# Optimization experiments

Hardware: AMD Instinct MI355X
Metric: run time of the kernel (lower is better)

Reference implementation:

```python
import jax, jax.numpy as jnp
import numpy as np


def _ln(x, w, b, eps):
    mu = jnp.mean(x, axis=-1, keepdims=True)
    var = jnp.mean((x - mu) ** 2, axis=-1, keepdims=True)
    return (x - mu) * jax.lax.rsqrt(var + eps) * w + b


def _conv(x, w, stride, groups):
    # x: (N, C, H, W), w: (O, C/groups, kh, kw), VALID padding, no bias
    return jax.lax.conv_general_dilated(
        x, w, window_strides=(stride, stride), padding='VALID',
        dimension_numbers=('NCHW', 'OIHW', 'NCHW'), feature_group_count=groups)


def setup_inputs() -> dict:
    key = jax.random.key(0)
    ks = jax.random.split(key, 8)
    B, Hp, Wp = 16, 56, 56
    d_c, d_v, H = 768, 768, 12
    t, kvp = 2, 4
    dh, dvh = d_c // H, d_v // H
    s = 0.02
    return {
        'x': jax.random.normal(ks[0], (B, Hp * Wp, d_c), jnp.float32),
        'patches_h': Hp,
        'patches_w': Wp,
        'norm_w': jnp.ones((d_c,), jnp.float32),
        'norm_b': jnp.zeros((d_c,), jnp.float32),
        'qkv_w': jax.random.normal(ks[1], (3 * d_c, d_c), jnp.float32) * s,
        'qkv_b': jnp.zeros((3 * d_c,), jnp.float32),
        'pool_q_w': jax.random.normal(ks[2], (dh, 1, t, t), jnp.float32) * s,
        'pool_k_w': jax.random.normal(ks[3], (dh, 1, kvp, kvp), jnp.float32) * s,
        'pool_v_w': jax.random.normal(ks[4], (dvh, dh, kvp, kvp), jnp.float32) * s,
        'normq_w': jnp.ones((dh,), jnp.float32),
        'normq_b': jnp.zeros((dh,), jnp.float32),
        'normk_w': jnp.ones((dh,), jnp.float32),
        'normk_b': jnp.zeros((dh,), jnp.float32),
        'normv_w': jnp.ones((dvh,), jnp.float32),
        'normv_b': jnp.zeros((dvh,), jnp.float32),
        'proj_w': jax.random.normal(ks[5], (d_v, d_v), jnp.float32) * s,
        'proj_b': jnp.zeros((d_v,), jnp.float32),
    }


def reference(x, patches_h, patches_w, norm_w, norm_b, qkv_w, qkv_b,
              pool_q_w, pool_k_w, pool_v_w, normq_w, normq_b,
              normk_w, normk_b, normv_w, normv_b, proj_w, proj_b):
    B, N_c, d_c = x.shape
    dh = pool_q_w.shape[0]
    H = d_c // dh
    dvh = pool_v_w.shape[0]
    d_v = dvh * H
    t = pool_q_w.shape[-1]
    kvp = pool_k_w.shape[-1]
    scale = dh ** -0.5

    xn = _ln(x, norm_w, norm_b, 1e-6)
    qkv = xn @ qkv_w.T + qkv_b                          # (B, N_c, 3*d_c)
    qkv = qkv.reshape(B, N_c, 3, H, dh).transpose(2, 0, 3, 1, 4)
    q, k, v = qkv[0], qkv[1], qkv[2]                     # (B, H, N_c, dh)

    def to_maps(a):
        return a.reshape(B * H, patches_h, patches_w, dh).transpose(0, 3, 1, 2)

    q = _conv(to_maps(q), pool_q_w, t, dh)               # (B*H, dh, Hp/t, Wp/t)
    k = _conv(to_maps(k), pool_k_w, kvp, dh)
    v = _conv(to_maps(v), pool_v_w, kvp, 1)              # (B*H, dvh, ., .)
    N_v = q.shape[-2] * q.shape[-1]
    N_kv = k.shape[-2] * k.shape[-1]

    # NOTE: raw row-major reshape, exactly matching torch's .reshape semantics
    q = _ln(q.reshape(B, H, N_v, dh), normq_w, normq_b, 1e-5)
    k = _ln(k.reshape(B, H, N_kv, dh), normk_w, normk_b, 1e-5)
    v = _ln(v.reshape(B, H, N_kv, dvh), normv_w, normv_b, 1e-5)

    attn = jax.nn.softmax(jnp.einsum('bhnd,bhmd->bhnm', q * scale, k), axis=-1)
    out = jnp.einsum('bhnm,bhmd->bhnd', attn, v)         # (B, H, N_v, dvh)
    out = out.transpose(0, 2, 1, 3).reshape(B, N_v, d_v)
    return out @ proj_w.T + proj_b
```

## Files before the change

kernel.cpp:

```cpp
#include <hip/hip_runtime.h>
#include <hip/hip_bf16.h>

using short8 = __attribute__((ext_vector_type(8))) short;
using f32x4  = __attribute__((ext_vector_type(4))) float;

#define DEVI __device__ __forceinline__
#define SWZ(byte, row) ((unsigned)(byte) ^ ((((unsigned)(row)) & 7u) << 4))

DEVI unsigned short f2bf(float f){
  unsigned int u = __float_as_uint(f);
  unsigned int r = (u + 0x7fffu + ((u >> 16) & 1u)) >> 16;
  return (unsigned short)r;
}
DEVI float bf2f(unsigned short u){ return __uint_as_float(((unsigned int)u) << 16); }

DEVI float wsum(float x){
  #pragma unroll
  for (int o = 32; o > 0; o >>= 1) x += __shfl_xor(x, o, 64);
  return x;
}

DEVI void async16(const void* g, void* l){
  __builtin_amdgcn_global_load_lds(
      (const __attribute__((address_space(1))) void*)g,
      (__attribute__((address_space(3))) void*)l,
      16, 0, 0);
}

__global__ void tobf16_kernel(const float* __restrict__ in, unsigned short* __restrict__ out, int n){
  int i = blockIdx.x * 256 + threadIdx.x;
  if (i < n) out[i] = f2bf(in[i]);
}

__global__ void conv_wv_kernel(const float* __restrict__ wv, unsigned short* __restrict__ wvb){
  int i = blockIdx.x * 256 + threadIdx.x;
  if (i >= 65536) return;
  int dv = i >> 10, c = (i >> 4) & 63, ij = i & 15;
  int y = ij >> 2, x = ij & 3;
  int pos = ((((y >> 1) & 1) * 2 + ((x >> 1) & 1)) << 2) + (y & 1) * 2 + (x & 1);
  wvb[dv * 1024 + pos * 64 + c] = f2bf(wv[i]);
}

__global__ __launch_bounds__(256)
void ln768_kernel(const float* __restrict__ x, const float* __restrict__ w,
                  const float* __restrict__ b, unsigned short* __restrict__ out)
{
  const int row  = blockIdx.x * 4 + (threadIdx.x >> 6);
  const int lane = threadIdx.x & 63;
  const float* xr = x + (size_t)row * 768;
  f32x4 v[3];
  float s = 0.f, s2 = 0.f;
  #pragma unroll
  for (int kk = 0; kk < 3; kk++){
    v[kk] = *(const f32x4*)&xr[lane * 4 + kk * 256];
    #pragma unroll
    for (int e = 0; e < 4; e++){ s += v[kk][e]; s2 += v[kk][e] * v[kk][e]; }
  }
  s = wsum(s); s2 = wsum(s2);
  float mu  = s * (1.f / 768.f);
  float var = s2 * (1.f / 768.f) - mu * mu;
  float rs  = rsqrtf(var + 1e-6f);

  const int bimg = row / 3136, tkn = row % 3136;
  const int y = tkn / 56, xx = tkn % 56;
  const int win = (y >> 2) * 14 + (xx >> 2);
  const int pos = ((((y >> 1) & 1) * 2 + ((xx >> 1) & 1)) << 2) + (y & 1) * 2 + (xx & 1);
  unsigned short* orow = out + ((size_t)bimg * 3136 + win * 16 + pos) * 768;

  #pragma unroll
  for (int kk = 0; kk < 3; kk++){
    int c0 = lane * 4 + kk * 256;
    float y0 = (v[kk][0] - mu) * rs * w[c0 + 0] + b[c0 + 0];
    float y1 = (v[kk][1] - mu) * rs * w[c0 + 1] + b[c0 + 1];
    float y2 = (v[kk][2] - mu) * rs * w[c0 + 2] + b[c0 + 2];
    float y3 = (v[kk][3] - mu) * rs * w[c0 + 3] + b[c0 + 3];
    unsigned int lo = (unsigned int)f2bf(y0) | ((unsigned int)f2bf(y1) << 16);
    unsigned int hi = (unsigned int)f2bf(y2) | ((unsigned int)f2bf(y3) << 16);
    *(uint2*)&orow[c0] = make_uint2(lo, hi);
  }
}

__global__ __launch_bounds__(256)
void ln64q_kernel(const float* __restrict__ in, const float* __restrict__ w,
                  const float* __restrict__ b, unsigned short* __restrict__ out)
{
  const size_t chunk = (size_t)blockIdx.x * 4 + (threadIdx.x >> 6);
  const int lane = threadIdx.x & 63;
  float xv = in[chunk * 64 + lane];
  float mu = wsum(xv) * (1.f / 64.f);
  float dl = xv - mu;
  float var = wsum(dl * dl) * (1.f / 64.f);
  float y = dl * rsqrtf(var + 1e-5f) * w[lane] + b[lane];
  out[chunk * 64 + lane] = f2bf(y * 0.125f);
}

__global__ __launch_bounds__(256)
void ln64k_kernel(const float* __restrict__ in, const float* __restrict__ w,
                  const float* __restrict__ b, unsigned short* __restrict__ Kb)
{
  const int chunk = blockIdx.x * 4 + (threadIdx.x >> 6);
  const int lane = threadIdx.x & 63;
  const int bh = chunk / 196, m = chunk % 196;
  float xv = in[(size_t)chunk * 64 + lane];
  float mu = wsum(xv) * (1.f / 64.f);
  float dl = xv - mu;
  float var = wsum(dl * dl) * (1.f / 64.f);
  float y = dl * rsqrtf(var + 1e-5f) * w[lane] + b[lane];
  char* og = (char*)Kb + (size_t)bh * 26624;
  *(unsigned short*)(og + SWZ(m * 128 + lane * 2, m)) = f2bf(y);
}

__global__ __launch_bounds__(256)
void vt_prep_kernel(const float* __restrict__ vpool, const float* __restrict__ w,
                    const float* __restrict__ b, unsigned short* __restrict__ Vtb)
{
  const int bh = blockIdx.x;
  __shared__ float Ls[196 * 65];
  const float* vb = vpool + (size_t)bh * 12544;
  const int t = threadIdx.x, lane = t & 63, wv = t >> 6;
  for (int i = t; i < 12544; i += 256){
    int n = i >> 6, d = i & 63;
    Ls[n * 65 + d] = vb[i];
  }
  __syncthreads();
  for (int n = wv; n < 196; n += 4){
    float xv = Ls[n * 65 + lane];
    float mu = wsum(xv) * (1.f / 64.f);
    float dl = xv - mu;
    float var = wsum(dl * dl) * (1.f / 64.f);
    Ls[n * 65 + lane] = dl * rsqrtf(var + 1e-5f) * w[lane] + b[lane];
  }
  __syncthreads();
  char* og = (char*)Vtb + (size_t)bh * 26624;
  for (int j = t; j < 12544; j += 256){
    int d = j / 196, n = j % 196;
    *(unsigned short*)(og + SWZ(d * 416 + n * 2, d)) = f2bf(Ls[n * 65 + d]);
  }
  for (int j = t; j < 768; j += 256){
    int d = j / 12, n = 196 + j % 12;
    *(unsigned short*)(og + SWZ(d * 416 + n * 2, d)) = 0;
  }
}

#define BAR() __builtin_amdgcn_s_barrier()
#define LGKM0() do{ asm volatile("s_waitcnt lgkmcnt(0)" ::: "memory"); __builtin_amdgcn_sched_barrier(0); }while(0)
#define VMW(N)  do{ asm volatile("s_waitcnt vmcnt(" #N ")" ::: "memory"); __builtin_amdgcn_sched_barrier(0); }while(0)

#define STAGE(GB, LOFF, KT, KS) do { \
  const unsigned short* gp_ = (GB) + (size_t)(KT) * 64 + (KS) * 32; \
  _Pragma("unroll") for (int l_ = 0; l_ < 2; ++l_){ \
    int i_ = l_ * 512 + tid; int row_ = i_ >> 2; int gch_ = (i_ & 3) ^ ((row_ >> 1) & 3); \
    async16(gp_ + (size_t)row_ * 768 + gch_ * 8, lds + (LOFF) + i_ * 16); \
  } } while(0)

#define LDA4(MH, KS) do { \
  _Pragma("unroll") for (int mm_ = 0; mm_ < 4; ++mm_){ \
    int row_ = wr * 128 + (MH) * 64 + mm_ * 16 + r; \
    Af[mm_] = *(const short8*)(lds + aoff + (KS) * 16384 + row_ * 64 + ((kg ^ ((row_ >> 1) & 3)) * 16)); \
  } } while(0)

#define LDB4(KS) do { \
  _Pragma("unroll") for (int nn_ = 0; nn_ < 4; ++nn_){ \
    int row_ = wc * 64 + nn_ * 16 + r; \
    Bf[nn_] = *(const short8*)(lds + boff + (KS) * 16384 + row_ * 64 + ((kg ^ ((row_ >> 1) & 3)) * 16)); \
  } } while(0)

#define MFMA16(MH) do { \
  __builtin_amdgcn_s_setprio(1); \
  _Pragma("unroll") for (int mm_ = 0; mm_ < 4; ++mm_) \
    _Pragma("unroll") for (int nn_ = 0; nn_ < 4; ++nn_) \
      acc[(MH) * 4 + mm_][nn_] = __builtin_amdgcn_mfma_f32_16x16x32_bf16(Af[mm_], Bf[nn_], acc[(MH) * 4 + mm_][nn_], 0, 0, 0); \
  __builtin_amdgcn_s_setprio(0); \
  } while(0)

__global__ __launch_bounds__(512, 2)
void gemm_qkv(const unsigned short* __restrict__ A, const unsigned short* __restrict__ W,
              const float* __restrict__ bias, const float* __restrict__ wq,
              const float* __restrict__ wk, float* __restrict__ qpool,
              float* __restrict__ kpool, unsigned short* __restrict__ vpart)
{
  constexpr int NT = 12;
  __shared__ __align__(128) char lds[131072];
  const int tid = threadIdx.x;
  const int lane = tid & 63, w = tid >> 6;
  const int r = lane & 15, kg = lane >> 4;
  const int wr = w >> 2, wc = w & 3;

  const int nwg = gridDim.x;
  const int lq = nwg >> 3, lr = nwg & 7;
  const int xcd = blockIdx.x & 7;
  const int wg = (xcd < lr ? xcd * (lq + 1) : lr * (lq + 1) + (xcd - lr) * lq) + (blockIdx.x >> 3);
  const int bm = wg / 9, bn = wg % 9;

  const unsigned short* Ag = A + (size_t)bm * 256 * 768;
  const unsigned short* Wg = W + (size_t)bn * 256 * 768;

  f32x4 acc[8][4];
  #pragma unroll
  for (int i = 0; i < 8; i++)
    #pragma unroll
    for (int j = 0; j < 4; j++) acc[i][j] = (f32x4){0.f, 0.f, 0.f, 0.f};

  STAGE(Ag, 0, 0, 0);
  STAGE(Wg, 65536, 0, 0);
  STAGE(Ag, 16384, 0, 1);
  STAGE(Wg, 65536 + 16384, 0, 1);
  STAGE(Ag, 32768, 1, 0);
  STAGE(Wg, 65536 + 32768, 1, 0);
  VMW(4); BAR();

  for (int t = 0; t < NT; ++t){
    const int slot = t & 1;
    const int aoff = slot * 32768;
    const int boff = 65536 + slot * 32768;
    const int sn1 = ((t + 1) & 1) * 32768;
    const bool st1 = (t + 1 < NT), st2 = (t + 2 < NT);
    short8 Af[4], Bf[4];

    LDB4(0); LDA4(0, 0);
    if (st1) STAGE(Ag, sn1 + 16384, t + 1, 1);
    BAR(); LGKM0();
    MFMA16(0);
    BAR();
    LDA4(1, 0);
    if (st1) STAGE(Wg, 65536 + sn1 + 16384, t + 1, 1);
    BAR(); LGKM0();
    MFMA16(1);
    BAR();
    LDB4(1); LDA4(0, 1);
    if (st2) STAGE(Ag, aoff, t + 2, 0);
    BAR(); LGKM0();
    MFMA16(0);
    BAR();
    LDA4(1, 1);
    if (st2) STAGE(Wg, 65536 + aoff, t + 2, 0);
    BAR(); LGKM0();
    MFMA16(1);
    if (t < NT - 2) { VMW(4); }
    else if (t == NT - 2) { VMW(0); }
    BAR();
  }

  const int region = bn / 3;
  const int hh = (bn % 3) * 4 + wc;
  const size_t gn0 = (size_t)bn * 256 + wc * 64;

  if (region == 2){
    const size_t m0 = (size_t)bm * 256 + wr * 128;
    #pragma unroll
    for (int m = 0; m < 8; m++){
      const size_t row = m0 + m * 16 + kg * 4;
      #pragma unroll
      for (int n = 0; n < 4; n++){
        const size_t col = (size_t)(bn % 3) * 256 + wc * 64 + n * 16 + r;
        const float bv = bias[gn0 + n * 16 + r];
        #pragma unroll
        for (int rg = 0; rg < 4; rg++)
          vpart[(row + rg) * 768 + col] = f2bf(acc[m][n][rg] + bv);
      }
    }
  } else if (region == 0){
    #pragma unroll
    for (int n = 0; n < 4; n++){
      const int c = n * 16 + r;
      const float bv = bias[gn0 + n * 16 + r];
      const float w0 = wq[c * 4 + 0], w1 = wq[c * 4 + 1];
      const float w2 = wq[c * 4 + 2], w3 = wq[c * 4 + 3];
      #pragma unroll
      for (int m = 0; m < 8; m++){
        int gw = bm * 16 + wr * 8 + m;
        int bimg = gw / 196, wir = gw - bimg * 196;
        int wy = wir / 14, wx = wir - wy * 14;
        float pooled = (acc[m][n][0] + bv) * w0 + (acc[m][n][1] + bv) * w1
                     + (acc[m][n][2] + bv) * w2 + (acc[m][n][3] + bv) * w3;
        int qy = 2 * wy + (kg >> 1), qx = 2 * wx + (kg & 1);
        qpool[((size_t)(bimg * 12 + hh)) * 50176 + (size_t)c * 784 + qy * 28 + qx] = pooled;
      }
    }
  } else {
    #pragma unroll
    for (int n = 0; n < 4; n++){
      const int c = n * 16 + r;
      const float bv = bias[gn0 + n * 16 + r];
      float wkr[4];
      #pragma unroll
      for (int rg = 0; rg < 4; rg++){
        int widx = ((kg >> 1) * 2 + (rg >> 1)) * 4 + (kg & 1) * 2 + (rg & 1);
        wkr[rg] = wk[c * 16 + widx];
      }
      #pragma unroll
      for (int m = 0; m < 8; m++){
        int gw = bm * 16 + wr * 8 + m;
        int bimg = gw / 196, wir = gw - bimg * 196;
        float part = (acc[m][n][0] + bv) * wkr[0] + (acc[m][n][1] + bv) * wkr[1]
                   + (acc[m][n][2] + bv) * wkr[2] + (acc[m][n][3] + bv) * wkr[3];
        part += __shfl_xor(part, 16, 64);
        part += __shfl_xor(part, 32, 64);
        if (kg == 0)
          kpool[((size_t)(bimg * 12 + hh)) * 12544 + (size_t)c * 196 + wir] = part;
      }
    }
  }
}

template <int OUT_BF16>
__global__ __launch_bounds__(256, 2)
void gemm_bt(const unsigned short* __restrict__ A, const unsigned short* __restrict__ W,
             const float* __restrict__ bias, void* __restrict__ Cout,
             int M, int N, int K)
{
  __shared__ short8 As8[512];
  __shared__ short8 Bs8[512];
  const int t = threadIdx.x;
  const int lane = t & 63;
  const int wv = t >> 6;
  const int wr = wv >> 1, wc = wv & 1;
  const int tiles_n = N >> 7;
  const int bm = blockIdx.x / tiles_n, bn = blockIdx.x % tiles_n;

  const unsigned short* Ag = A + (size_t)bm * 128 * K;
  const unsigned short* Wg = W + (size_t)bn * 128 * K;

  f32x4 acc[4][4];
  #pragma unroll
  for (int i = 0; i < 4; i++)
    #pragma unroll
    for (int j = 0; j < 4; j++) acc[i][j] = (f32x4){0.f, 0.f, 0.f, 0.f};

  const int r = lane & 15, kg = lane >> 4;

  for (int kt = 0; kt < K; kt += 32){
    #pragma unroll
    for (int j = 0; j < 2; j++){
      int c = j * 256 + t;
      int row = c >> 2, kc = c & 3;
      async16(Ag + (size_t)row * K + kt + kc * 8, &As8[c]);
      async16(Wg + (size_t)row * K + kt + kc * 8, &Bs8[c]);
    }
    __syncthreads();
    short8 af[4], bfr[4];
    #pragma unroll
    for (int mi = 0; mi < 4; mi++) af[mi] = As8[(wr * 64 + mi * 16 + r) * 4 + kg];
    #pragma unroll
    for (int ni = 0; ni < 4; ni++) bfr[ni] = Bs8[(wc * 64 + ni * 16 + r) * 4 + kg];
    #pragma unroll
    for (int mi = 0; mi < 4; mi++)
      #pragma unroll
      for (int ni = 0; ni < 4; ni++)
        acc[mi][ni] = __builtin_amdgcn_mfma_f32_16x16x32_bf16(af[mi], bfr[ni], acc[mi][ni], 0, 0, 0);
    __syncthreads();
  }

  const size_t m0 = (size_t)bm * 128 + wr * 64;
  const size_t n0 = (size_t)bn * 128 + wc * 64;
  #pragma unroll
  for (int mi = 0; mi < 4; mi++){
    #pragma unroll
    for (int ni = 0; ni < 4; ni++){
      size_t row = m0 + mi * 16 + kg * 4;
      size_t col = n0 + ni * 16 + r;
      float bvv = bias[col];
      #pragma unroll
      for (int rg = 0; rg < 4; rg++){
        float val = acc[mi][ni][rg] + bvv;
        if (OUT_BF16) ((unsigned short*)Cout)[(row + rg) * N + col] = f2bf(val);
        else          ((float*)Cout)[(row + rg) * N + col] = val;
      }
    }
  }
}

__global__ __launch_bounds__(256)
void pool_v_kernel(const unsigned short* __restrict__ vpart, const unsigned short* __restrict__ wvb,
                   float* __restrict__ out)
{
  const int bid = blockIdx.x;
  const int bh = bid / 14, wy = bid % 14;
  const int b = bh / 12, h = bh % 12;
  __shared__ __align__(128) char Alds[14 * 2048];
  const int t = threadIdx.x, lane = t & 63, w = t >> 6;
  const int r = lane & 15, kg = lane >> 4;

  #pragma unroll
  for (int l = 0; l < 7; l++){
    int j = l * 256 + t;
    int win = j >> 7, s = j & 127;
    int gch = s ^ (win & 7);
    int p = gch >> 3, c8 = gch & 7;
    const unsigned short* src = vpart + ((size_t)(b * 3136 + (wy * 14 + win) * 16 + p)) * 768 + h * 64 + c8 * 8;
    async16(src, Alds + j * 16);
  }
  __syncthreads();

  f32x4 acc = (f32x4){0.f, 0.f, 0.f, 0.f};
  const int dv = w * 16 + r;
  #pragma unroll 4
  for (int kt = 0; kt < 1024; kt += 32){
    int ck = (kt >> 3) + kg;
    short8 af = *(const short8*)(Alds + r * 2048 + ((ck ^ (r & 7)) * 16));
    short8 bfr = *(const short8*)&wvb[(size_t)dv * 1024 + kt + kg * 8];
    acc = __builtin_amdgcn_mfma_f32_16x16x32_bf16(af, bfr, acc, 0, 0, 0);
  }
  #pragma unroll
  for (int rg = 0; rg < 4; rg++){
    int wx = kg * 4 + rg;
    if (wx < 14)
      out[(size_t)bh * 12544 + (size_t)dv * 196 + wy * 14 + wx] = acc[rg];
  }
}

__global__ __launch_bounds__(256)
void attn2_kernel(const unsigned short* __restrict__ Qb, const unsigned short* __restrict__ Kb,
                  const unsigned short* __restrict__ Vtb, unsigned short* __restrict__ out)
{
  const int bid = blockIdx.x;
  const int bh = bid / 13, qt = bid % 13;
  const int b = bh / 12, h = bh % 12;
  __shared__ __align__(128) char K_lds[26624];
  __shared__ __align__(128) char V_lds[26624];
  __shared__ __align__(128) char P_lds[26624];
  const int t = threadIdx.x, lane = t & 63, w = t >> 6;
  const int r = lane & 15, kg = lane >> 4;
  const short8 z8 = {0, 0, 0, 0, 0, 0, 0, 0};

  const char* Kg = (const char*)Kb + (size_t)bh * 26624;
  const char* Vg = (const char*)Vtb + (size_t)bh * 26624;
  #pragma unroll
  for (int i = 0; i < 7; i++){
    int j = i * 256 + t;
    if (j < 1664) async16(Kg + j * 16, K_lds + j * 16);
  }
  #pragma unroll
  for (int i = 0; i < 7; i++){
    int j = i * 256 + t;
    if (j < 1664) async16(Vg + j * 16, V_lds + j * 16);
  }

  const size_t qrow = (size_t)bh * 784 + qt * 64 + w * 16 + r;
  short8 aq0 = *(const short8*)&Qb[qrow * 64 + kg * 8];
  short8 aq1 = *(const short8*)&Qb[qrow * 64 + 32 + kg * 8];

  __syncthreads();

  f32x4 s[13];
  #pragma unroll
  for (int nf = 0; nf < 13; nf++){
    int row = nf * 16 + r;
    short8 bk0 = *(const short8*)(K_lds + SWZ(row * 128 + kg * 16, row));
    short8 bk1 = *(const short8*)(K_lds + SWZ(row * 128 + 64 + kg * 16, row));
    f32x4 a = (f32x4){0.f, 0.f, 0.f, 0.f};
    a = __builtin_amdgcn_mfma_f32_16x16x32_bf16(aq0, bk0, a, 0, 0, 0);
    a = __builtin_amdgcn_mfma_f32_16x16x32_bf16(aq1, bk1, a, 0, 0, 0);
    s[nf] = a;
  }

  #pragma unroll
  for (int rg = 0; rg < 4; rg++) if (r >= 4) s[12][rg] = -1e30f;

  float inv[4];
  #pragma unroll
  for (int rg = 0; rg < 4; rg++){
    float m0 = s[0][rg];
    #pragma unroll
    for (int nf = 1; nf < 13; nf++) m0 = fmaxf(m0, s[nf][rg]);
    m0 = fmaxf(m0, __shfl_xor(m0, 1, 64));
    m0 = fmaxf(m0, __shfl_xor(m0, 2, 64));
    m0 = fmaxf(m0, __shfl_xor(m0, 4, 64));
    m0 = fmaxf(m0, __shfl_xor(m0, 8, 64));
    const int q = w * 16 + kg * 4 + rg;
    float sum = 0.f;
    #pragma unroll
    for (int nf = 0; nf < 13; nf++){
      float p = __expf(s[nf][rg] - m0);
      if (nf == 12 && r >= 4) p = 0.f;
      sum += p;
      *(unsigned short*)(P_lds + SWZ(q * 416 + (nf * 16 + r) * 2, q)) = f2bf(p);
    }
    sum += __shfl_xor(sum, 1, 64);
    sum += __shfl_xor(sum, 2, 64);
    sum += __shfl_xor(sum, 4, 64);
    sum += __shfl_xor(sum, 8, 64);
    inv[rg] = 1.f / sum;
  }

  f32x4 o[4];
  #pragma unroll
  for (int i = 0; i < 4; i++) o[i] = (f32x4){0.f, 0.f, 0.f, 0.f};
  const int qr = w * 16 + r;
  #pragma unroll
  for (int ks = 0; ks < 7; ks++){
    short8 ap = z8, bv0 = z8, bv1 = z8, bv2 = z8, bv3 = z8;
    if (ks < 6 || kg < 2){
      ap  = *(const short8*)(P_lds + SWZ(qr * 416 + ks * 64 + kg * 16, qr));
      bv0 = *(const short8*)(V_lds + SWZ((0 * 16 + r) * 416 + ks * 64 + kg * 16, (0 * 16 + r)));
      bv1 = *(const short8*)(V_lds + SWZ((1 * 16 + r) * 416 + ks * 64 + kg * 16, (1 * 16 + r)));
      bv2 = *(const short8*)(V_lds + SWZ((2 * 16 + r) * 416 + ks * 64 + kg * 16, (2 * 16 + r)));
      bv3 = *(const short8*)(V_lds + SWZ((3 * 16 + r) * 416 + ks * 64 + kg * 16, (3 * 16 + r)));
    }
    o[0] = __builtin_amdgcn_mfma_f32_16x16x32_bf16(ap, bv0, o[0], 0, 0, 0);
    o[1] = __builtin_amdgcn_mfma_f32_16x16x32_bf16(ap, bv1, o[1], 0, 0, 0);
    o[2] = __builtin_amdgcn_mfma_f32_16x16x32_bf16(ap, bv2, o[2], 0, 0, 0);
    o[3] = __builtin_amdgcn_mfma_f32_16x16x32_bf16(ap, bv3, o[3], 0, 0, 0);
  }

  #pragma unroll
  for (int rg = 0; rg < 4; rg++){
    int qg = qt * 64 + w * 16 + kg * 4 + rg;
    if (qg < 784){
      unsigned short* orow = out + ((size_t)b * 784 + qg) * 768 + h * 64;
      float sc = inv[rg];
      orow[ 0 + r] = f2bf(o[0][rg] * sc);
      orow[16 + r] = f2bf(o[1][rg] * sc);
      orow[32 + r] = f2bf(o[2][rg] * sc);
      orow[48 + r] = f2bf(o[3][rg] * sc);
    }
  }
}

extern "C" void kernel_launch(void* const* d_in, const int* in_sizes, int n_in,
                              void* d_out, int out_size, void* d_ws, size_t ws_size,
                              hipStream_t stream)
{
  (void)in_sizes; (void)n_in; (void)out_size; (void)ws_size;
  const float* x      = (const float*)d_in[0];
  const float* norm_w = (const float*)d_in[3];
  const float* norm_b = (const float*)d_in[4];
  const float* qkv_w  = (const float*)d_in[5];
  const float* qkv_b  = (const float*)d_in[6];
  const float* pq_w   = (const float*)d_in[7];
  const float* pk_w   = (const float*)d_in[8];
  const float* pv_w   = (const float*)d_in[9];
  const float* nq_w   = (const float*)d_in[10];
  const float* nq_b   = (const float*)d_in[11];
  const float* nk_w   = (const float*)d_in[12];
  const float* nk_b   = (const float*)d_in[13];
  const float* nv_w   = (const float*)d_in[14];
  const float* nv_b   = (const float*)d_in[15];
  const float* proj_w = (const float*)d_in[16];
  const float* proj_b = (const float*)d_in[17];
  float* outp = (float*)d_out;

  char* ws = (char*)d_ws;
  size_t o = 0;
  unsigned short* wqkv16  = (unsigned short*)(ws + o); o += 3538944;
  unsigned short* wproj16 = (unsigned short*)(ws + o); o += 1179648;
  unsigned short* wv16    = (unsigned short*)(ws + o); o += 131072;
  char* xn_region         = (ws + o);                  o += 77070336;
  unsigned short* vpart   = (unsigned short*)(ws + o); o += 77070336;
  float*  qpool           = (float*)(ws + o);          o += 38535168;
  float*  kpool           = (float*)(ws + o);          o += 9633792;
  float*  vpool           = (float*)(ws + o);          o += 9633792;
  unsigned short* attno   = (unsigned short*)(ws + o); o += 19267584;

  unsigned short* xn  = (unsigned short*)xn_region;
  unsigned short* Qb  = (unsigned short*)xn_region;
  unsigned short* Kbt = (unsigned short*)(xn_region + 19275776);
  unsigned short* Vtb = (unsigned short*)(xn_region + 19275776 + 5111808);

  tobf16_kernel<<<(1769472 + 255) / 256, 256, 0, stream>>>(qkv_w, wqkv16, 1769472);
  tobf16_kernel<<<(589824 + 255) / 256, 256, 0, stream>>>(proj_w, wproj16, 589824);
  conv_wv_kernel<<<256, 256, 0, stream>>>(pv_w, wv16);

  ln768_kernel<<<12544, 256, 0, stream>>>(x, norm_w, norm_b, xn);

  gemm_qkv<<<196 * 9, 512, 0, stream>>>(xn, wqkv16, qkv_b, pq_w, pk_w, qpool, kpool, vpart);

  pool_v_kernel<<<192 * 14, 256, 0, stream>>>(vpart, wv16, vpool);

  ln64q_kernel<<<150528 / 4, 256, 0, stream>>>(qpool, nq_w, nq_b, Qb);
  ln64k_kernel<<<37632 / 4, 256, 0, stream>>>(kpool, nk_w, nk_b, Kbt);
  vt_prep_kernel<<<192, 256, 0, stream>>>(vpool, nv_w, nv_b, Vtb);

  attn2_kernel<<<192 * 13, 256, 0, stream>>>(Qb, Kbt, Vtb, attno);

  gemm_bt<0><<<98 * 6, 256, 0, stream>>>(attno, wproj16, proj_b, outp, 12544, 768, 768);
}
```

Measured before the change: 423.2 us.

## Fuse V pooling conv into QKV GEMM epilogue and Q layernorm into attention

```diff
diff --git a/kernel.cpp b/kernel.cpp
--- a/kernel.cpp
+++ b/kernel.cpp
@@ -78,20 +78,6 @@
     unsigned int hi = (unsigned int)f2bf(y2) | ((unsigned int)f2bf(y3) << 16);
     *(uint2*)&orow[c0] = make_uint2(lo, hi);
   }
-}
-
-__global__ __launch_bounds__(256)
-void ln64q_kernel(const float* __restrict__ in, const float* __restrict__ w,
-                  const float* __restrict__ b, unsigned short* __restrict__ out)
-{
-  const size_t chunk = (size_t)blockIdx.x * 4 + (threadIdx.x >> 6);
-  const int lane = threadIdx.x & 63;
-  float xv = in[chunk * 64 + lane];
-  float mu = wsum(xv) * (1.f / 64.f);
-  float dl = xv - mu;
-  float var = wsum(dl * dl) * (1.f / 64.f);
-  float y = dl * rsqrtf(var + 1e-5f) * w[lane] + b[lane];
-  out[chunk * 64 + lane] = f2bf(y * 0.125f);
 }
 
 __global__ __launch_bounds__(256)
@@ -176,8 +162,9 @@
 __global__ __launch_bounds__(512, 2)
 void gemm_qkv(const unsigned short* __restrict__ A, const unsigned short* __restrict__ W,
               const float* __restrict__ bias, const float* __restrict__ wq,
-              const float* __restrict__ wk, float* __restrict__ qpool,
-              float* __restrict__ kpool, unsigned short* __restrict__ vpart)
+              const float* __restrict__ wk, const unsigned short* __restrict__ wvb,
+              float* __restrict__ qpool, float* __restrict__ kpool,
+              float* __restrict__ vpool)
 {
   constexpr int NT = 12;
   __shared__ __align__(128) char lds[131072];
@@ -246,17 +233,41 @@
   const size_t gn0 = (size_t)bn * 256 + wc * 64;
 
   if (region == 2){
-    const size_t m0 = (size_t)bm * 256 + wr * 128;
     #pragma unroll
     for (int m = 0; m < 8; m++){
-      const size_t row = m0 + m * 16 + kg * 4;
+      const int win = wr * 8 + m;
       #pragma unroll
       for (int n = 0; n < 4; n++){
-        const size_t col = (size_t)(bn % 3) * 256 + wc * 64 + n * 16 + r;
+        const int c = n * 16 + r;
         const float bv = bias[gn0 + n * 16 + r];
         #pragma unroll
-        for (int rg = 0; rg < 4; rg++)
-          vpart[(row + rg) * 768 + col] = f2bf(acc[m][n][rg] + bv);
+        for (int rg = 0; rg < 4; rg++){
+          const int pos = kg * 4 + rg;
+          const int chs = (pos * 8 + (c >> 3)) ^ (win & 7);
+          *(unsigned short*)(lds + wc * 32768 + win * 2048 + chs * 16 + (c & 7) * 2)
+              = f2bf(acc[m][n][rg] + bv);
+        }
+      }
+    }
+    BAR();
+    const int hh2 = (bn % 3) * 4 + (w & 3);
+    const char* Av = lds + (w & 3) * 32768;
+    #pragma unroll
+    for (int dg = 0; dg < 2; dg++){
+      const int dvg = (w >> 2) * 2 + dg;
+      f32x4 a2 = (f32x4){0.f, 0.f, 0.f, 0.f};
+      #pragma unroll 4
+      for (int kt = 0; kt < 1024; kt += 32){
+        int ck = (kt >> 3) + kg;
+        short8 af = *(const short8*)(Av + r * 2048 + ((ck ^ (r & 7)) * 16));
+        short8 bfr = *(const short8*)&wvb[(size_t)(dvg * 16 + r) * 1024 + kt + kg * 8];
+        a2 = __builtin_amdgcn_mfma_f32_16x16x32_bf16(af, bfr, a2, 0, 0, 0);
+      }
+      #pragma unroll
+      for (int rg = 0; rg < 4; rg++){
+        int gw = bm * 16 + kg * 4 + rg;
+        int bimg = gw / 196, wir = gw - bimg * 196;
+        vpool[((size_t)(bimg * 12 + hh2)) * 12544 + (size_t)(dvg * 16 + r) * 196 + wir] = a2[rg];
       }
     }
   } else if (region == 0){
@@ -371,46 +382,8 @@
 }
 
 __global__ __launch_bounds__(256)
-void pool_v_kernel(const unsigned short* __restrict__ vpart, const unsigned short* __restrict__ wvb,
-                   float* __restrict__ out)
-{
-  const int bid = blockIdx.x;
-  const int bh = bid / 14, wy = bid % 14;
-  const int b = bh / 12, h = bh % 12;
-  __shared__ __align__(128) char Alds[14 * 2048];
-  const int t = threadIdx.x, lane = t & 63, w = t >> 6;
-  const int r = lane & 15, kg = lane >> 4;
-
-  #pragma unroll
-  for (int l = 0; l < 7; l++){
-    int j = l * 256 + t;
-    int win = j >> 7, s = j & 127;
-    int gch = s ^ (win & 7);
-    int p = gch >> 3, c8 = gch & 7;
-    const unsigned short* src = vpart + ((size_t)(b * 3136 + (wy * 14 + win) * 16 + p)) * 768 + h * 64 + c8 * 8;
-    async16(src, Alds + j * 16);
-  }
-  __syncthreads();
-
-  f32x4 acc = (f32x4){0.f, 0.f, 0.f, 0.f};
-  const int dv = w * 16 + r;
-  #pragma unroll 4
-  for (int kt = 0; kt < 1024; kt += 32){
-    int ck = (kt >> 3) + kg;
-    short8 af = *(const short8*)(Alds + r * 2048 + ((ck ^ (r & 7)) * 16));
-    short8 bfr = *(const short8*)&wvb[(size_t)dv * 1024 + kt + kg * 8];
-    acc = __builtin_amdgcn_mfma_f32_16x16x32_bf16(af, bfr, acc, 0, 0, 0);
-  }
-  #pragma unroll
-  for (int rg = 0; rg < 4; rg++){
-    int wx = kg * 4 + rg;
-    if (wx < 14)
-      out[(size_t)bh * 12544 + (size_t)dv * 196 + wy * 14 + wx] = acc[rg];
-  }
-}
-
-__global__ __launch_bounds__(256)
-void attn2_kernel(const unsigned short* __restrict__ Qb, const unsigned short* __restrict__ Kb,
+void attn2_kernel(const float* __restrict__ qpool, const float* __restrict__ nqw,
+                  const float* __restrict__ nqb, const unsigned short* __restrict__ Kb,
                   const unsigned short* __restrict__ Vtb, unsigned short* __restrict__ out)
 {
   const int bid = blockIdx.x;
@@ -436,9 +409,34 @@
     if (j < 1664) async16(Vg + j * 16, V_lds + j * 16);
   }
 
-  const size_t qrow = (size_t)bh * 784 + qt * 64 + w * 16 + r;
-  short8 aq0 = *(const short8*)&Qb[qrow * 64 + kg * 8];
-  short8 aq1 = *(const short8*)&Qb[qrow * 64 + 32 + kg * 8];
+  const float* qpr = qpool + (size_t)bh * 50176 + (size_t)(qt * 64 + w * 16 + r) * 64;
+  f32x4 qv[4];
+  qv[0] = *(const f32x4*)&qpr[kg * 8];
+  qv[1] = *(const f32x4*)&qpr[kg * 8 + 4];
+  qv[2] = *(const f32x4*)&qpr[32 + kg * 8];
+  qv[3] = *(const f32x4*)&qpr[32 + kg * 8 + 4];
+  float s1 = 0.f, s2 = 0.f;
+  #pragma unroll
+  for (int i = 0; i < 4; i++)
+    #pragma unroll
+    for (int e = 0; e < 4; e++){ s1 += qv[i][e]; s2 += qv[i][e] * qv[i][e]; }
+  s1 += __shfl_xor(s1, 16, 64); s1 += __shfl_xor(s1, 32, 64);
+  s2 += __shfl_xor(s2, 16, 64); s2 += __shfl_xor(s2, 32, 64);
+  const float mu = s1 * (1.f / 64.f);
+  const float rs = rsqrtf(s2 * (1.f / 64.f) - mu * mu + 1e-5f);
+  f32x4 lw[4], lb[4];
+  lw[0] = *(const f32x4*)&nqw[kg * 8];      lw[1] = *(const f32x4*)&nqw[kg * 8 + 4];
+  lw[2] = *(const f32x4*)&nqw[32 + kg * 8]; lw[3] = *(const f32x4*)&nqw[32 + kg * 8 + 4];
+  lb[0] = *(const f32x4*)&nqb[kg * 8];      lb[1] = *(const f32x4*)&nqb[kg * 8 + 4];
+  lb[2] = *(const f32x4*)&nqb[32 + kg * 8]; lb[3] = *(const f32x4*)&nqb[32 + kg * 8 + 4];
+  short8 aq0, aq1;
+  #pragma unroll
+  for (int j = 0; j < 8; j++){
+    float y0 = ((qv[j >> 2][j & 3] - mu) * rs * lw[j >> 2][j & 3] + lb[j >> 2][j & 3]) * 0.125f;
+    float y1 = ((qv[2 + (j >> 2)][j & 3] - mu) * rs * lw[2 + (j >> 2)][j & 3] + lb[2 + (j >> 2)][j & 3]) * 0.125f;
+    aq0[j] = (short)f2bf(y0);
+    aq1[j] = (short)f2bf(y1);
+  }
 
   __syncthreads();
 
@@ -546,14 +544,12 @@
   unsigned short* wproj16 = (unsigned short*)(ws + o); o += 1179648;
   unsigned short* wv16    = (unsigned short*)(ws + o); o += 131072;
   char* xn_region         = (ws + o);                  o += 77070336;
-  unsigned short* vpart   = (unsigned short*)(ws + o); o += 77070336;
   float*  qpool           = (float*)(ws + o);          o += 38535168;
   float*  kpool           = (float*)(ws + o);          o += 9633792;
   float*  vpool           = (float*)(ws + o);          o += 9633792;
   unsigned short* attno   = (unsigned short*)(ws + o); o += 19267584;
 
   unsigned short* xn  = (unsigned short*)xn_region;
-  unsigned short* Qb  = (unsigned short*)xn_region;
   unsigned short* Kbt = (unsigned short*)(xn_region + 19275776);
   unsigned short* Vtb = (unsigned short*)(xn_region + 19275776 + 5111808);
 
@@ -563,15 +559,13 @@
 
   ln768_kernel<<<12544, 256, 0, stream>>>(x, norm_w, norm_b, xn);
 
-  gemm_qkv<<<196 * 9, 512, 0, stream>>>(xn, wqkv16, qkv_b, pq_w, pk_w, qpool, kpool, vpart);
-
-  pool_v_kernel<<<192 * 14, 256, 0, stream>>>(vpart, wv16, vpool);
-
-  ln64q_kernel<<<150528 / 4, 256, 0, stream>>>(qpool, nq_w, nq_b, Qb);
+  gemm_qkv<<<196 * 9, 512, 0, stream>>>(xn, wqkv16, qkv_b, pq_w, pk_w, wv16,
+                                        qpool, kpool, vpool);
+
   ln64k_kernel<<<37632 / 4, 256, 0, stream>>>(kpool, nk_w, nk_b, Kbt);
   vt_prep_kernel<<<192, 256, 0, stream>>>(vpool, nv_w, nv_b, Vtb);
 
-  attn2_kernel<<<192 * 13, 256, 0, stream>>>(Qb, Kbt, Vtb, attno);
+  attn2_kernel<<<192 * 13, 256, 0, stream>>>(qpool, nq_w, nq_b, Kbt, Vtb, attno);
 
   gemm_bt<0><<<98 * 6, 256, 0, stream>>>(attno, wproj16, proj_b, outp, 12544, 768, 768);
 }
```

Measured after the change: 401.3 us. 5.2% less time.
